# Optimization experiments

Measured on AMD Instinct MI355X. Metric: run time of the kernel, lower is better.

The kernel has to match this reference:

```python
import jax, jax.numpy as jnp
import numpy as np

B, T, F, H, C = 32, 512, 512, 1024, 1000


def setup_inputs() -> dict:
    key = jax.random.key(0)
    ks = jax.random.split(key, 9)
    return {
        "data": jax.random.normal(ks[0], (B, T, F), dtype=jnp.float32),
        "h0": jax.random.normal(ks[1], (H,), dtype=jnp.float32),
        "c0": jax.random.normal(ks[2], (H,), dtype=jnp.float32),
        "w_f": jax.random.normal(ks[3], (H + F, H), dtype=jnp.float32),
        "w_i": jax.random.normal(ks[4], (H + F, H), dtype=jnp.float32),
        "w_c1": jax.random.normal(ks[5], (H + F, H), dtype=jnp.float32),
        "w_o": jax.random.normal(ks[6], (H + F, H), dtype=jnp.float32),
        "fc_w": jax.random.normal(ks[7], (C, H), dtype=jnp.float32),
        "fc_b": jax.random.normal(ks[8], (C,), dtype=jnp.float32),
    }


def reference(data, h0, c0, w_f, w_i, w_c1, w_o, fc_w, fc_b):
    b, t, _ = data.shape
    h = h0.shape[0]
    # Original module never updates h0/c0 inside the time loop, so every
    # timestep sees the same initial state; vectorize gates over time.
    z = jnp.concatenate([jnp.broadcast_to(h0, (b, t, h)), data], axis=-1)  # [B,T,H+F]
    # Stack the 4 gate weights into one fused matmul: [H+F, 4H]
    w_all = jnp.concatenate([w_f, w_i, w_c1, w_o], axis=1)
    g = jnp.einsum('btz,zk->btk', z, w_all)  # [B,T,4H]
    f_g, i_g, c1_g, o_g = jnp.split(g, 4, axis=-1)
    f_g = jax.nn.sigmoid(f_g)
    i_g = jax.nn.sigmoid(i_g)
    c1_g = jnp.tanh(c1_g)
    o_g = jax.nn.sigmoid(o_g)
    c = f_g * c0 + i_g * c1_g          # [B,T,H]
    h_all = o_g * jnp.tanh(c)          # [B,T,H]
    h_last = h_all[:, -1]              # output depends on last timestep only
    logits = jax.nn.relu(h_last @ fc_w.T + fc_b)
    return jax.nn.log_softmax(logits, axis=1)
```

## Files before the change

### kernel.cpp

```cpp
#include <hip/hip_runtime.h>
#include <math.h>

#define BB 32
#define TT 512
#define FF 512
#define HH 1024
#define CC 1000
#define QQ (4*HH)
#define FCB 8
#define KCN 8
#define KS  (HH/KCN)

template<int JCH, int CHH, int JCD, int CHD>
__global__ __launch_bounds__(512, 4) void k_gates(
    const float* __restrict__ data, const float* __restrict__ h0,
    const float* __restrict__ wf, const float* __restrict__ wi,
    const float* __restrict__ wc, const float* __restrict__ wo,
    float* __restrict__ hp, float* __restrict__ dp)
{
    constexpr int LDSN = (BB*JCD > JCH) ? BB*JCD : JCH;
    __shared__ float lds[LDSN];
    const int t  = threadIdx.x;
    const int bx = blockIdx.x;
    constexpr int NH0 = 2*CHH;

    if (bx < NH0) {
        const int cb2 = bx & 1;
        const int ch  = bx >> 1;
        const int q   = cb2*2048 + t*4;
        const int gate = q >> 10;
        const int k4   = q & (HH-1);
        const float* w = (gate==0) ? wf : (gate==1) ? wi : (gate==2) ? wc : wo;
        if (t < JCH) lds[t] = h0[ch*JCH + t];
        __syncthreads();
        float4 s = make_float4(0.f,0.f,0.f,0.f);
        #pragma unroll
        for (int j = 0; j < JCH; j += 4) {
            const float4 w0 = *(const float4*)(w + (size_t)(ch*JCH + j+0)*HH + k4);
            const float4 w1 = *(const float4*)(w + (size_t)(ch*JCH + j+1)*HH + k4);
            const float4 w2 = *(const float4*)(w + (size_t)(ch*JCH + j+2)*HH + k4);
            const float4 w3 = *(const float4*)(w + (size_t)(ch*JCH + j+3)*HH + k4);
            const float h0v = lds[j+0], h1v = lds[j+1], h2v = lds[j+2], h3v = lds[j+3];
            s.x += h0v*w0.x; s.y += h0v*w0.y; s.z += h0v*w0.z; s.w += h0v*w0.w;
            s.x += h1v*w1.x; s.y += h1v*w1.y; s.z += h1v*w1.z; s.w += h1v*w1.w;
            s.x += h2v*w2.x; s.y += h2v*w2.y; s.z += h2v*w2.z; s.w += h2v*w2.w;
            s.x += h3v*w3.x; s.y += h3v*w3.y; s.z += h3v*w3.z; s.w += h3v*w3.w;
        }
        *(float4*)(hp + (size_t)ch*QQ + q) = s;
    } else {
        const int idx  = bx - NH0;
        const int cb   = idx & 15;
        const int cd   = idx >> 4;
        const int q0   = cb*256;
        const int gate = q0 >> 10;
        const int k0   = q0 & (HH-1);
        const float* w = (gate==0) ? wf : (gate==1) ? wi : (gate==2) ? wc : wo;
        const int jc0  = cd*JCD;

        for (int s = t; s < BB*JCD/4; s += 512) {
            const int b  = s / (JCD/4);
            const int jj = (s % (JCD/4))*4;
            const float4 v = *(const float4*)(data + (size_t)b*TT*FF + (size_t)(TT-1)*FF + jc0 + jj);
            lds[b*JCD + jj+0] = v.x; lds[b*JCD + jj+1] = v.y;
            lds[b*JCD + jj+2] = v.z; lds[b*JCD + jj+3] = v.w;
        }
        __syncthreads();

        const int c4 = t & 63;
        const int b0 = (t >> 6) * 4;
        const int k4 = k0 + c4*4;
        float4 acc[4];
        #pragma unroll
        for (int bi = 0; bi < 4; ++bi) acc[bi] = make_float4(0.f,0.f,0.f,0.f);

        #pragma unroll 2
        for (int j = 0; j < JCD; j += 4) {
            const float4 w0 = *(const float4*)(w + (size_t)(HH + jc0 + j+0)*HH + k4);
            const float4 w1 = *(const float4*)(w + (size_t)(HH + jc0 + j+1)*HH + k4);
            const float4 w2 = *(const float4*)(w + (size_t)(HH + jc0 + j+2)*HH + k4);
            const float4 w3 = *(const float4*)(w + (size_t)(HH + jc0 + j+3)*HH + k4);
            #pragma unroll
            for (int bi = 0; bi < 4; ++bi) {
                const float d0 = lds[(b0+bi)*JCD + j+0];
                const float d1 = lds[(b0+bi)*JCD + j+1];
                const float d2 = lds[(b0+bi)*JCD + j+2];
                const float d3 = lds[(b0+bi)*JCD + j+3];
                acc[bi].x += d0*w0.x; acc[bi].y += d0*w0.y; acc[bi].z += d0*w0.z; acc[bi].w += d0*w0.w;
                acc[bi].x += d1*w1.x; acc[bi].y += d1*w1.y; acc[bi].z += d1*w1.z; acc[bi].w += d1*w1.w;
                acc[bi].x += d2*w2.x; acc[bi].y += d2*w2.y; acc[bi].z += d2*w2.z; acc[bi].w += d2*w2.w;
                acc[bi].x += d3*w3.x; acc[bi].y += d3*w3.y; acc[bi].z += d3*w3.z; acc[bi].w += d3*w3.w;
            }
        }
        #pragma unroll
        for (int bi = 0; bi < 4; ++bi)
            *(float4*)(dp + ((size_t)cd*BB + b0 + bi)*QQ + q0 + c4*4) = acc[bi];
    }
}

template<int CH, int CD>
__global__ __launch_bounds__(256, 2) void k_cell(
    const float* __restrict__ hp, const float* __restrict__ dp,
    const float* __restrict__ c0, float* __restrict__ hlast)
{
    __shared__ float4 p[4][64];
    const int t    = threadIdx.x;
    const int kblk = blockIdx.x;
    const int b    = blockIdx.y;
    const int g    = t >> 6;
    const int i    = t & 63;
    const int q    = g*HH + kblk*256 + i*4;

    float4 s = make_float4(0.f,0.f,0.f,0.f);
    #pragma unroll 8
    for (int ch = 0; ch < CH; ++ch) {
        const float4 v = *(const float4*)(hp + (size_t)ch*QQ + q);
        s.x += v.x; s.y += v.y; s.z += v.z; s.w += v.w;
    }
    #pragma unroll 8
    for (int cd = 0; cd < CD; ++cd) {
        const float4 v = *(const float4*)(dp + ((size_t)cd*BB + b)*QQ + q);
        s.x += v.x; s.y += v.y; s.z += v.z; s.w += v.w;
    }
    p[g][i] = s;
    __syncthreads();

    if (t < 64) {
        const float4 gf = p[0][t], gi = p[1][t], gc = p[2][t], go = p[3][t];
        const float4 cv = *(const float4*)(c0 + kblk*256 + t*4);
        float4 h;
        { const float f=1.f/(1.f+expf(-gf.x)), ii=1.f/(1.f+expf(-gi.x)), cg=tanhf(gc.x), o=1.f/(1.f+expf(-go.x)); h.x=o*tanhf(f*cv.x+ii*cg); }
        { const float f=1.f/(1.f+expf(-gf.y)), ii=1.f/(1.f+expf(-gi.y)), cg=tanhf(gc.y), o=1.f/(1.f+expf(-go.y)); h.y=o*tanhf(f*cv.y+ii*cg); }
        { const float f=1.f/(1.f+expf(-gf.z)), ii=1.f/(1.f+expf(-gi.z)), cg=tanhf(gc.z), o=1.f/(1.f+expf(-go.z)); h.z=o*tanhf(f*cv.z+ii*cg); }
        { const float f=1.f/(1.f+expf(-gf.w)), ii=1.f/(1.f+expf(-gi.w)), cg=tanhf(gc.w), o=1.f/(1.f+expf(-go.w)); h.w=o*tanhf(f*cv.w+ii*cg); }
        *(float4*)(hlast + (size_t)b*HH + kblk*256 + t*4) = h;
    }
}

__global__ __launch_bounds__(256) void k_fc_part(
    const float* __restrict__ hlast, const float* __restrict__ fcw,
    float* __restrict__ pl)
{
    __shared__ float hs[BB][KS+2];
    __shared__ float wl[FCB][KS+2];
    const int t  = threadIdx.x;
    const int c0 = blockIdx.x * FCB;
    const int kc = blockIdx.y;
    const int k0 = kc*KS;
    const int b  = t & 31;
    const int cl = t >> 5;
    const int c  = c0 + cl;

    for (int l = t; l < BB*(KS/4); l += 256) {
        const int bb = l >> 5, kk = l & 31;
        const float4 v = *(const float4*)(hlast + (size_t)bb*HH + k0 + kk*4);
        *(float2*)&hs[bb][kk*4+0] = make_float2(v.x, v.y);
        *(float2*)&hs[bb][kk*4+2] = make_float2(v.z, v.w);
    }
    for (int l = t; l < FCB*(KS/4); l += 256) {
        const int cc = l >> 5, kk = l & 31;
        const float4 v = *(const float4*)(fcw + (size_t)(c0+cc)*HH + k0 + kk*4);
        *(float2*)&wl[cc][kk*4+0] = make_float2(v.x, v.y);
        *(float2*)&wl[cc][kk*4+2] = make_float2(v.z, v.w);
    }
    __syncthreads();

    float acc = 0.f;
    #pragma unroll 16
    for (int k2 = 0; k2 < KS/2; ++k2) {
        const float2 h2 = *(const float2*)&hs[b][k2*2];
        const float2 w2 = *(const float2*)&wl[cl][k2*2];
        acc += h2.x*w2.x + h2.y*w2.y;
    }
    pl[((size_t)kc*BB + b)*CC + c] = acc;
}

__global__ __launch_bounds__(256) void k_lsm(
    const float* __restrict__ pl, const float* __restrict__ fcb,
    float* __restrict__ out)
{
    __shared__ float red[8];
    const int b = blockIdx.x, t = threadIdx.x;
    float v[4]; float vmax = -1e30f;
    #pragma unroll
    for (int ci = 0; ci < 4; ++ci) {
        const int c = t + ci*256;
        if (c < CC) {
            float s = fcb[c];
            #pragma unroll
            for (int kc = 0; kc < KCN; ++kc)
                s += pl[((size_t)kc*BB + b)*CC + c];
            v[ci] = fmaxf(s, 0.f);
            vmax = fmaxf(vmax, v[ci]);
        } else v[ci] = -1e30f;
    }
    for (int o = 32; o > 0; o >>= 1) vmax = fmaxf(vmax, __shfl_down(vmax, o, 64));
    const int lane = t & 63, wid = t >> 6;
    if (lane == 0) red[wid] = vmax;
    __syncthreads();
    if (t == 0) red[4] = fmaxf(fmaxf(red[0], red[1]), fmaxf(red[2], red[3]));
    __syncthreads();
    const float m = red[4];
    float se = 0.f;
    #pragma unroll
    for (int ci = 0; ci < 4; ++ci) {
        const int c = t + ci*256;
        if (c < CC) se += expf(v[ci] - m);
    }
    for (int o = 32; o > 0; o >>= 1) se += __shfl_down(se, o, 64);
    if (lane == 0) red[wid] = se;
    __syncthreads();
    if (t == 0) red[5] = m + logf(red[0] + red[1] + red[2] + red[3]);
    __syncthreads();
    const float lse = red[5];
    #pragma unroll
    for (int ci = 0; ci < 4; ++ci) {
        const int c = t + ci*256;
        if (c < CC) out[(size_t)b*CC + c] = v[ci] - lse;
    }
}

extern "C" void kernel_launch(void* const* d_in, const int* in_sizes, int n_in,
                              void* d_out, int out_size, void* d_ws, size_t ws_size,
                              hipStream_t stream) {
    const float* data = (const float*)d_in[0];
    const float* h0   = (const float*)d_in[1];
    const float* c0   = (const float*)d_in[2];
    const float* wf   = (const float*)d_in[3];
    const float* wi   = (const float*)d_in[4];
    const float* wc   = (const float*)d_in[5];
    const float* wo   = (const float*)d_in[6];
    const float* fcw  = (const float*)d_in[7];
    const float* fcb  = (const float*)d_in[8];
    float* out = (float*)d_out;

    const size_t needA = ((size_t)32*QQ + (size_t)16*BB*QQ + (size_t)BB*HH + (size_t)KCN*BB*CC) * 4;
    const bool cfgA = (ws_size >= needA);

    float* ws = (float*)d_ws;
    if (cfgA) {
        float* hp = ws;
        float* dp = hp + (size_t)32*QQ;
        float* hl = dp + (size_t)16*BB*QQ;
        float* pl = hl + (size_t)BB*HH;
        k_gates<32,32,32,16><<<dim3(2*32 + 16*16), 512, 0, stream>>>(data, h0, wf, wi, wc, wo, hp, dp);
        k_cell<32,16><<<dim3(HH/256, BB), 256, 0, stream>>>(hp, dp, c0, hl);
        k_fc_part<<<dim3(CC/FCB, KCN), 256, 0, stream>>>(hl, fcw, pl);
        k_lsm<<<dim3(BB), 256, 0, stream>>>(pl, fcb, out);
    } else {
        float* hp = ws;
        float* dp = hp + (size_t)32*QQ;
        float* hl = dp + (size_t)4*BB*QQ;
        float* pl = hl + (size_t)BB*HH;
        k_gates<32,32,128,4><<<dim3(2*32 + 16*4), 512, 0, stream>>>(data, h0, wf, wi, wc, wo, hp, dp);
        k_cell<32,4><<<dim3(HH/256, BB), 256, 0, stream>>>(hp, dp, c0, hl);
        k_fc_part<<<dim3(CC/FCB, KCN), 256, 0, stream>>>(hl, fcw, pl);
        k_lsm<<<dim3(BB), 256, 0, stream>>>(pl, fcb, out);
    }
}
```

Measured before the change: 31.74 us.

## Fuse LSTM cell activation with FC partial products and widen softmax block

Merges the cell-activation kernel and the FC partial-product kernel so each block computes a 256-wide slice of h for one batch row in shared memory and immediately multiplies it against the FC weights. This removes one launch and the global round trip of h_last, and halves the K-split for the FC reduction. The log-softmax kernel uses 1024 threads with one class per thread. In exchange, each FC weight row is now re-read per batch row, greatly multiplying weight traffic and duplicating cell reductions across the class split.

Result: slower. 32.74 us (+3.2%).

```diff
diff --git a/kernel.cpp b/kernel.cpp
--- a/kernel.cpp
+++ b/kernel.cpp
@@ -7,9 +7,7 @@
 #define HH 1024
 #define CC 1000
 #define QQ (4*HH)
-#define FCB 8
-#define KCN 8
-#define KS  (HH/KCN)
+#define KCN 4
 
 template<int JCH, int CHH, int JCD, int CHD>
 __global__ __launch_bounds__(512, 4) void k_gates(
@@ -98,17 +96,20 @@
 }
 
 template<int CH, int CD>
-__global__ __launch_bounds__(256, 2) void k_cell(
+__global__ __launch_bounds__(256, 2) void k_cellfc(
     const float* __restrict__ hp, const float* __restrict__ dp,
-    const float* __restrict__ c0, float* __restrict__ hlast)
+    const float* __restrict__ c0, const float* __restrict__ fcw,
+    float* __restrict__ pl)
 {
     __shared__ float4 p[4][64];
-    const int t    = threadIdx.x;
-    const int kblk = blockIdx.x;
-    const int b    = blockIdx.y;
-    const int g    = t >> 6;
-    const int i    = t & 63;
-    const int q    = g*HH + kblk*256 + i*4;
+    __shared__ __align__(16) float hl_s[256];
+    const int t  = threadIdx.x;
+    const int kc = blockIdx.x;
+    const int b  = blockIdx.y;
+    const int cz = blockIdx.z;
+    const int g  = t >> 6;
+    const int i  = t & 63;
+    const int q  = g*HH + kc*256 + i*4;
 
     float4 s = make_float4(0.f,0.f,0.f,0.f);
     #pragma unroll 8
@@ -125,98 +126,77 @@
     __syncthreads();
 
     if (t < 64) {
-        const float4 gf = p[0][t], gi = p[1][t], gc = p[2][t], go = p[3][t];
-        const float4 cv = *(const float4*)(c0 + kblk*256 + t*4);
+        const float4 gf = p[0][t], gi4 = p[1][t], gc = p[2][t], go = p[3][t];
+        const float4 cv = *(const float4*)(c0 + kc*256 + t*4);
         float4 h;
-        { const float f=1.f/(1.f+expf(-gf.x)), ii=1.f/(1.f+expf(-gi.x)), cg=tanhf(gc.x), o=1.f/(1.f+expf(-go.x)); h.x=o*tanhf(f*cv.x+ii*cg); }
-        { const float f=1.f/(1.f+expf(-gf.y)), ii=1.f/(1.f+expf(-gi.y)), cg=tanhf(gc.y), o=1.f/(1.f+expf(-go.y)); h.y=o*tanhf(f*cv.y+ii*cg); }
-        { const float f=1.f/(1.f+expf(-gf.z)), ii=1.f/(1.f+expf(-gi.z)), cg=tanhf(gc.z), o=1.f/(1.f+expf(-go.z)); h.z=o*tanhf(f*cv.z+ii*cg); }
-        { const float f=1.f/(1.f+expf(-gf.w)), ii=1.f/(1.f+expf(-gi.w)), cg=tanhf(gc.w), o=1.f/(1.f+expf(-go.w)); h.w=o*tanhf(f*cv.w+ii*cg); }
-        *(float4*)(hlast + (size_t)b*HH + kblk*256 + t*4) = h;
-    }
-}
-
-__global__ __launch_bounds__(256) void k_fc_part(
-    const float* __restrict__ hlast, const float* __restrict__ fcw,
-    float* __restrict__ pl)
-{
-    __shared__ float hs[BB][KS+2];
-    __shared__ float wl[FCB][KS+2];
-    const int t  = threadIdx.x;
-    const int c0 = blockIdx.x * FCB;
-    const int kc = blockIdx.y;
-    const int k0 = kc*KS;
-    const int b  = t & 31;
-    const int cl = t >> 5;
-    const int c  = c0 + cl;
-
-    for (int l = t; l < BB*(KS/4); l += 256) {
-        const int bb = l >> 5, kk = l & 31;
-        const float4 v = *(const float4*)(hlast + (size_t)bb*HH + k0 + kk*4);
-        *(float2*)&hs[bb][kk*4+0] = make_float2(v.x, v.y);
-        *(float2*)&hs[bb][kk*4+2] = make_float2(v.z, v.w);
-    }
-    for (int l = t; l < FCB*(KS/4); l += 256) {
-        const int cc = l >> 5, kk = l & 31;
-        const float4 v = *(const float4*)(fcw + (size_t)(c0+cc)*HH + k0 + kk*4);
-        *(float2*)&wl[cc][kk*4+0] = make_float2(v.x, v.y);
-        *(float2*)&wl[cc][kk*4+2] = make_float2(v.z, v.w);
-    }
-    __syncthreads();
-
-    float acc = 0.f;
-    #pragma unroll 16
-    for (int k2 = 0; k2 < KS/2; ++k2) {
-        const float2 h2 = *(const float2*)&hs[b][k2*2];
-        const float2 w2 = *(const float2*)&wl[cl][k2*2];
-        acc += h2.x*w2.x + h2.y*w2.y;
-    }
-    pl[((size_t)kc*BB + b)*CC + c] = acc;
-}
-
-__global__ __launch_bounds__(256) void k_lsm(
+        { const float f=1.f/(1.f+expf(-gf.x)), ii=1.f/(1.f+expf(-gi4.x)), cg=tanhf(gc.x), o=1.f/(1.f+expf(-go.x)); h.x=o*tanhf(f*cv.x+ii*cg); }
+        { const float f=1.f/(1.f+expf(-gf.y)), ii=1.f/(1.f+expf(-gi4.y)), cg=tanhf(gc.y), o=1.f/(1.f+expf(-go.y)); h.y=o*tanhf(f*cv.y+ii*cg); }
+        { const float f=1.f/(1.f+expf(-gf.z)), ii=1.f/(1.f+expf(-gi4.z)), cg=tanhf(gc.z), o=1.f/(1.f+expf(-go.z)); h.z=o*tanhf(f*cv.z+ii*cg); }
+        { const float f=1.f/(1.f+expf(-gf.w)), ii=1.f/(1.f+expf(-gi4.w)), cg=tanhf(gc.w), o=1.f/(1.f+expf(-go.w)); h.w=o*tanhf(f*cv.w+ii*cg); }
+        *(float4*)&hl_s[t*4] = h;
+    }
+    __syncthreads();
+
+    const int gi = t >> 3;
+    const int l8 = t & 7;
+    for (int m = cz*16; m < cz*16 + 16; ++m) {
+        const int c = m*32 + gi;
+        if (c < CC) {
+            const float4* wr = (const float4*)(fcw + (size_t)c*HH + kc*256);
+            float acc = 0.f;
+            #pragma unroll
+            for (int m8 = 0; m8 < 8; ++m8) {
+                const float4 w4 = wr[l8 + m8*8];
+                const float4 h4 = *(const float4*)&hl_s[(l8 + m8*8)*4];
+                acc += w4.x*h4.x + w4.y*h4.y + w4.z*h4.z + w4.w*h4.w;
+            }
+            acc += __shfl_xor(acc, 1, 64);
+            acc += __shfl_xor(acc, 2, 64);
+            acc += __shfl_xor(acc, 4, 64);
+            if (l8 == 0) pl[((size_t)kc*BB + b)*CC + c] = acc;
+        }
+    }
+}
+
+__global__ __launch_bounds__(1024) void k_lsm(
     const float* __restrict__ pl, const float* __restrict__ fcb,
     float* __restrict__ out)
 {
-    __shared__ float red[8];
+    __shared__ float red[20];
     const int b = blockIdx.x, t = threadIdx.x;
-    float v[4]; float vmax = -1e30f;
-    #pragma unroll
-    for (int ci = 0; ci < 4; ++ci) {
-        const int c = t + ci*256;
-        if (c < CC) {
-            float s = fcb[c];
-            #pragma unroll
-            for (int kc = 0; kc < KCN; ++kc)
-                s += pl[((size_t)kc*BB + b)*CC + c];
-            v[ci] = fmaxf(s, 0.f);
-            vmax = fmaxf(vmax, v[ci]);
-        } else v[ci] = -1e30f;
-    }
-    for (int o = 32; o > 0; o >>= 1) vmax = fmaxf(vmax, __shfl_down(vmax, o, 64));
-    const int lane = t & 63, wid = t >> 6;
-    if (lane == 0) red[wid] = vmax;
-    __syncthreads();
-    if (t == 0) red[4] = fmaxf(fmaxf(red[0], red[1]), fmaxf(red[2], red[3]));
-    __syncthreads();
-    const float m = red[4];
-    float se = 0.f;
-    #pragma unroll
-    for (int ci = 0; ci < 4; ++ci) {
-        const int c = t + ci*256;
-        if (c < CC) se += expf(v[ci] - m);
-    }
-    for (int o = 32; o > 0; o >>= 1) se += __shfl_down(se, o, 64);
-    if (lane == 0) red[wid] = se;
-    __syncthreads();
-    if (t == 0) red[5] = m + logf(red[0] + red[1] + red[2] + red[3]);
-    __syncthreads();
-    const float lse = red[5];
-    #pragma unroll
-    for (int ci = 0; ci < 4; ++ci) {
-        const int c = t + ci*256;
-        if (c < CC) out[(size_t)b*CC + c] = v[ci] - lse;
-    }
+    const int w = t >> 6, l = t & 63;
+    float v = -1e30f;
+    if (t < CC) {
+        float s = fcb[t];
+        #pragma unroll
+        for (int kc = 0; kc < KCN; ++kc)
+            s += pl[((size_t)kc*BB + b)*CC + t];
+        v = fmaxf(s, 0.f);
+    }
+    float m = v;
+    for (int o = 32; o > 0; o >>= 1) m = fmaxf(m, __shfl_xor(m, o, 64));
+    if (l == 0) red[w] = m;
+    __syncthreads();
+    if (t == 0) {
+        float mm = red[0];
+        #pragma unroll
+        for (int ww = 1; ww < 16; ++ww) mm = fmaxf(mm, red[ww]);
+        red[16] = mm;
+    }
+    __syncthreads();
+    const float mb = red[16];
+    float se = (t < CC) ? expf(v - mb) : 0.f;
+    for (int o = 32; o > 0; o >>= 1) se += __shfl_xor(se, o, 64);
+    if (l == 0) red[w] = se;
+    __syncthreads();
+    if (t == 0) {
+        float ss = 0.f;
+        #pragma unroll
+        for (int ww = 0; ww < 16; ++ww) ss += red[ww];
+        red[17] = mb + logf(ss);
+    }
+    __syncthreads();
+    if (t < CC) out[(size_t)b*CC + t] = v - red[17];
 }
 
 extern "C" void kernel_launch(void* const* d_in, const int* in_sizes, int n_in,
@@ -233,27 +213,23 @@
     const float* fcb  = (const float*)d_in[8];
     float* out = (float*)d_out;
 
-    const size_t needA = ((size_t)32*QQ + (size_t)16*BB*QQ + (size_t)BB*HH + (size_t)KCN*BB*CC) * 4;
+    const size_t needA = ((size_t)32*QQ + (size_t)16*BB*QQ + (size_t)KCN*BB*CC) * 4;
     const bool cfgA = (ws_size >= needA);
 
     float* ws = (float*)d_ws;
     if (cfgA) {
         float* hp = ws;
         float* dp = hp + (size_t)32*QQ;
-        float* hl = dp + (size_t)16*BB*QQ;
-        float* pl = hl + (size_t)BB*HH;
+        float* pl = dp + (size_t)16*BB*QQ;
         k_gates<32,32,32,16><<<dim3(2*32 + 16*16), 512, 0, stream>>>(data, h0, wf, wi, wc, wo, hp, dp);
-        k_cell<32,16><<<dim3(HH/256, BB), 256, 0, stream>>>(hp, dp, c0, hl);
-        k_fc_part<<<dim3(CC/FCB, KCN), 256, 0, stream>>>(hl, fcw, pl);
-        k_lsm<<<dim3(BB), 256, 0, stream>>>(pl, fcb, out);
+        k_cellfc<32,16><<<dim3(KCN, BB, 2), 256, 0, stream>>>(hp, dp, c0, fcw, pl);
+        k_lsm<<<dim3(BB), 1024, 0, stream>>>(pl, fcb, out);
     } else {
         float* hp = ws;
         float* dp = hp + (size_t)32*QQ;
-        float* hl = dp + (size_t)4*BB*QQ;
-        float* pl = hl + (size_t)BB*HH;
+        float* pl = dp + (size_t)4*BB*QQ;
         k_gates<32,32,128,4><<<dim3(2*32 + 16*4), 512, 0, stream>>>(data, h0, wf, wi, wc, wo, hp, dp);
-        k_cell<32,4><<<dim3(HH/256, BB), 256, 0, stream>>>(hp, dp, c0, hl);
-        k_fc_part<<<dim3(CC/FCB, KCN), 256, 0, stream>>>(hl, fcw, pl);
-        k_lsm<<<dim3(BB), 256, 0, stream>>>(pl, fcb, out);
-    }
-}
+        k_cellfc<32,4><<<dim3(KCN, BB, 2), 256, 0, stream>>>(hp, dp, c0, fcw, pl);
+        k_lsm<<<dim3(BB), 1024, 0, stream>>>(pl, fcb, out);
+    }
+}
```

## Split gate GEMV work across more blocks with in-block LDS reduction

Applied to the files above, without the earlier changes.

The h0 part of the gate computation now splits each 32-row chunk across 4 thread groups of 8 rows each, with a shared-memory reduction. Each block also covers fewer output columns, so four times as many blocks are launched. The data part halves the column tile and the batch rows per thread, doubling its block count. The aim is more blocks and more memory-level parallelism for a bandwidth-bound weight stream, at the cost of an extra sync, LDS traffic, and less register reuse of the data values.

New measurement: 31.65 us. No clear change (-0.3%).

```diff
diff --git a/kernel.cpp b/kernel.cpp
--- a/kernel.cpp
+++ b/kernel.cpp
@@ -11,47 +11,62 @@
 #define KCN 8
 #define KS  (HH/KCN)
 
-template<int JCH, int CHH, int JCD, int CHD>
+template<int CHH, int JCD, int CHD>
 __global__ __launch_bounds__(512, 4) void k_gates(
     const float* __restrict__ data, const float* __restrict__ h0,
     const float* __restrict__ wf, const float* __restrict__ wi,
     const float* __restrict__ wc, const float* __restrict__ wo,
     float* __restrict__ hp, float* __restrict__ dp)
 {
-    constexpr int LDSN = (BB*JCD > JCH) ? BB*JCD : JCH;
-    __shared__ float lds[LDSN];
+    constexpr int LDSH = 32 + 4*128*4;
+    constexpr int LDSN = (BB*JCD > LDSH) ? BB*JCD : LDSH;
+    __shared__ __align__(16) float lds[LDSN];
     const int t  = threadIdx.x;
     const int bx = blockIdx.x;
-    constexpr int NH0 = 2*CHH;
+    constexpr int NH0 = 8*CHH;
 
     if (bx < NH0) {
-        const int cb2 = bx & 1;
-        const int ch  = bx >> 1;
-        const int q   = cb2*2048 + t*4;
-        const int gate = q >> 10;
-        const int k4   = q & (HH-1);
+        const int cb8 = bx & 7;
+        const int ch  = bx >> 3;
+        const int q0  = cb8*512;
+        const int gate = q0 >> 10;
+        const int k0   = q0 & (HH-1);
         const float* w = (gate==0) ? wf : (gate==1) ? wi : (gate==2) ? wc : wo;
-        if (t < JCH) lds[t] = h0[ch*JCH + t];
+        if (t < 32) lds[t] = h0[ch*32 + t];
         __syncthreads();
+        const int lane = t & 127;
+        const int rg   = t >> 7;
+        const int k4   = k0 + lane*4;
+        const int j0   = rg*8;
         float4 s = make_float4(0.f,0.f,0.f,0.f);
         #pragma unroll
-        for (int j = 0; j < JCH; j += 4) {
-            const float4 w0 = *(const float4*)(w + (size_t)(ch*JCH + j+0)*HH + k4);
-            const float4 w1 = *(const float4*)(w + (size_t)(ch*JCH + j+1)*HH + k4);
-            const float4 w2 = *(const float4*)(w + (size_t)(ch*JCH + j+2)*HH + k4);
-            const float4 w3 = *(const float4*)(w + (size_t)(ch*JCH + j+3)*HH + k4);
-            const float h0v = lds[j+0], h1v = lds[j+1], h2v = lds[j+2], h3v = lds[j+3];
+        for (int j = 0; j < 8; j += 4) {
+            const float4 w0 = *(const float4*)(w + (size_t)(ch*32 + j0 + j+0)*HH + k4);
+            const float4 w1 = *(const float4*)(w + (size_t)(ch*32 + j0 + j+1)*HH + k4);
+            const float4 w2 = *(const float4*)(w + (size_t)(ch*32 + j0 + j+2)*HH + k4);
+            const float4 w3 = *(const float4*)(w + (size_t)(ch*32 + j0 + j+3)*HH + k4);
+            const float h0v = lds[j0+j+0], h1v = lds[j0+j+1];
+            const float h2v = lds[j0+j+2], h3v = lds[j0+j+3];
             s.x += h0v*w0.x; s.y += h0v*w0.y; s.z += h0v*w0.z; s.w += h0v*w0.w;
             s.x += h1v*w1.x; s.y += h1v*w1.y; s.z += h1v*w1.z; s.w += h1v*w1.w;
             s.x += h2v*w2.x; s.y += h2v*w2.y; s.z += h2v*w2.z; s.w += h2v*w2.w;
             s.x += h3v*w3.x; s.y += h3v*w3.y; s.z += h3v*w3.z; s.w += h3v*w3.w;
         }
-        *(float4*)(hp + (size_t)ch*QQ + q) = s;
+        float4* pg = (float4*)(lds + 32);
+        pg[rg*128 + lane] = s;
+        __syncthreads();
+        if (t < 128) {
+            const float4 a0 = pg[t], a1 = pg[128+t], a2 = pg[256+t], a3 = pg[384+t];
+            float4 r;
+            r.x = a0.x+a1.x+a2.x+a3.x; r.y = a0.y+a1.y+a2.y+a3.y;
+            r.z = a0.z+a1.z+a2.z+a3.z; r.w = a0.w+a1.w+a2.w+a3.w;
+            *(float4*)(hp + (size_t)ch*QQ + q0 + t*4) = r;
+        }
     } else {
         const int idx  = bx - NH0;
-        const int cb   = idx & 15;
-        const int cd   = idx >> 4;
-        const int q0   = cb*256;
+        const int cb   = idx & 31;
+        const int cd   = idx >> 5;
+        const int q0   = cb*128;
         const int gate = q0 >> 10;
         const int k0   = q0 & (HH-1);
         const float* w = (gate==0) ? wf : (gate==1) ? wi : (gate==2) ? wc : wo;
@@ -66,12 +81,12 @@
         }
         __syncthreads();
 
-        const int c4 = t & 63;
-        const int b0 = (t >> 6) * 4;
+        const int c4 = t & 31;
+        const int b0 = (t >> 5) * 2;
         const int k4 = k0 + c4*4;
-        float4 acc[4];
-        #pragma unroll
-        for (int bi = 0; bi < 4; ++bi) acc[bi] = make_float4(0.f,0.f,0.f,0.f);
+        float4 acc[2];
+        acc[0] = make_float4(0.f,0.f,0.f,0.f);
+        acc[1] = make_float4(0.f,0.f,0.f,0.f);
 
         #pragma unroll 2
         for (int j = 0; j < JCD; j += 4) {
@@ -80,7 +95,7 @@
             const float4 w2 = *(const float4*)(w + (size_t)(HH + jc0 + j+2)*HH + k4);
             const float4 w3 = *(const float4*)(w + (size_t)(HH + jc0 + j+3)*HH + k4);
             #pragma unroll
-            for (int bi = 0; bi < 4; ++bi) {
+            for (int bi = 0; bi < 2; ++bi) {
                 const float d0 = lds[(b0+bi)*JCD + j+0];
                 const float d1 = lds[(b0+bi)*JCD + j+1];
                 const float d2 = lds[(b0+bi)*JCD + j+2];
@@ -92,7 +107,7 @@
             }
         }
         #pragma unroll
-        for (int bi = 0; bi < 4; ++bi)
+        for (int bi = 0; bi < 2; ++bi)
             *(float4*)(dp + ((size_t)cd*BB + b0 + bi)*QQ + q0 + c4*4) = acc[bi];
     }
 }
@@ -242,7 +257,7 @@
         float* dp = hp + (size_t)32*QQ;
         float* hl = dp + (size_t)16*BB*QQ;
         float* pl = hl + (size_t)BB*HH;
-        k_gates<32,32,32,16><<<dim3(2*32 + 16*16), 512, 0, stream>>>(data, h0, wf, wi, wc, wo, hp, dp);
+        k_gates<32,32,16><<<dim3(8*32 + 32*16), 512, 0, stream>>>(data, h0, wf, wi, wc, wo, hp, dp);
         k_cell<32,16><<<dim3(HH/256, BB), 256, 0, stream>>>(hp, dp, c0, hl);
         k_fc_part<<<dim3(CC/FCB, KCN), 256, 0, stream>>>(hl, fcw, pl);
         k_lsm<<<dim3(BB), 256, 0, stream>>>(pl, fcb, out);
@@ -251,7 +266,7 @@
         float* dp = hp + (size_t)32*QQ;
         float* hl = dp + (size_t)4*BB*QQ;
         float* pl = hl + (size_t)BB*HH;
-        k_gates<32,32,128,4><<<dim3(2*32 + 16*4), 512, 0, stream>>>(data, h0, wf, wi, wc, wo, hp, dp);
+        k_gates<32,128,4><<<dim3(8*32 + 32*4), 512, 0, stream>>>(data, h0, wf, wi, wc, wo, hp, dp);
         k_cell<32,4><<<dim3(HH/256, BB), 256, 0, stream>>>(hp, dp, c0, hl);
         k_fc_part<<<dim3(CC/FCB, KCN), 256, 0, stream>>>(hl, fcw, pl);
         k_lsm<<<dim3(BB), 256, 0, stream>>>(pl, fcb, out);
```
